# Optimization experiments

Hardware: AMD Instinct MI355X
Metric: run time of the kernel (lower is better)

The kernel has to match this reference:

```python
import jax, jax.numpy as jnp
import numpy as np

APERTURE = 256
IGNORE_ITSELF = False
FMAX = jnp.float32(3.4028235e38)  # tf.float32.max


def setup_inputs() -> dict:
    key = jax.random.key(0)
    ks = jax.random.split(key, 5)
    n, m, d = 4096, 1024, 1024
    scale = 1.0 / np.sqrt(m)
    x = jax.random.normal(ks[0], (n, m), dtype=jnp.float32)
    WK = jax.random.normal(ks[1], (m, d), dtype=jnp.float32) * scale
    WQ = jax.random.normal(ks[2], (m, d), dtype=jnp.float32) * scale
    WV = jax.random.normal(ks[3], (m, d), dtype=jnp.float32) * scale
    Wout = jax.random.normal(ks[4], (d, m), dtype=jnp.float32) * scale
    return {"x": x, "WK": WK, "WQ": WQ, "WV": WV, "Wout": Wout}


def reference(x, WK, WQ, WV, Wout):
    n = x.shape[0]
    K = x @ WK                      # [n, d]
    Q = (x @ WQ) * 0.06             # [n, d]
    V = x @ WV                      # [n, d]
    logits = Q @ K.T                # [n, n]

    i = jnp.arange(n)[:, None]
    j = jnp.arange(n)[None, :]
    if IGNORE_ITSELF:
        keep = (i != j).astype(jnp.float32)
        logits = logits * keep - FMAX * (1.0 - keep)
    if APERTURE > 0:
        # tf: mask = 1 - band_part(ones, -aperture, aperture); negative num_lower
        # keeps the whole lower triangle, so mask==1 exactly where j - i > aperture.
        keep = (j - i > APERTURE).astype(jnp.float32)
        logits = logits * keep - FMAX * (1.0 - keep)

    att_weights = jax.nn.softmax(logits, axis=-1)  # [n, n]
    # dropout is identity (training=False). NOTE faithful quirk: transpose_a=True.
    y = att_weights.T @ V           # [n, d]
    y = y @ Wout                    # [n, m]
    return (y, att_weights)
```

## Files before the change

### kernel.cpp

```cpp
#include <hip/hip_runtime.h>
#include <cstdint>
#include <cstddef>

#define N_TOK 4096
#define M_DIM 1024
#define APER  256
#define UNIF_START 3839

typedef __attribute__((ext_vector_type(8))) short short8;
typedef __attribute__((ext_vector_type(4))) float float4_t;

__device__ __forceinline__ unsigned short f2bf(float x) {
    union { float f; uint32_t u; } v; v.f = x;
    uint32_t u = v.u;
    u += 0x7FFFu + ((u >> 16) & 1u);
    return (unsigned short)(u >> 16);
}

__device__ __forceinline__ void gload16(const void* g, void* l) {
    __builtin_amdgcn_global_load_lds(
        (const __attribute__((address_space(1))) void*)g,
        (__attribute__((address_space(3))) void*)l, 16, 0, 0);
}

__global__ __launch_bounds__(256) void cast_bf16(const float* __restrict__ src,
                                                 unsigned short* __restrict__ dst, int n) {
    const int i = (blockIdx.x * 256 + threadIdx.x) * 4;
    if (i >= n) return;
    const float4 v = *reinterpret_cast<const float4*>(&src[i]);
    ushort4 o;
    o.x = f2bf(v.x); o.y = f2bf(v.y); o.z = f2bf(v.z); o.w = f2bf(v.w);
    *reinterpret_cast<ushort4*>(&dst[i]) = o;
}

__global__ __launch_bounds__(256) void wtrans3(const float* __restrict__ W0, const float* __restrict__ W1,
                                               const float* __restrict__ W2,
                                               unsigned short* __restrict__ D0, unsigned short* __restrict__ D1,
                                               unsigned short* __restrict__ D2) {
    const int z = blockIdx.z;
    const float* src = z == 0 ? W0 : (z == 1 ? W1 : W2);
    unsigned short* dst = z == 0 ? D0 : (z == 1 ? D1 : D2);
    __shared__ unsigned short tile[32][33];
    const int c0 = blockIdx.x * 32, r0 = blockIdx.y * 32;
    const int tx = threadIdx.x & 31, ty = threadIdx.x >> 5;
#pragma unroll
    for (int i = ty; i < 32; i += 8)
        tile[i][tx] = f2bf(src[(size_t)(r0 + i) * M_DIM + c0 + tx]);
    __syncthreads();
#pragma unroll
    for (int i = ty; i < 32; i += 8)
        dst[(size_t)(c0 + i) * M_DIM + r0 + tx] = tile[tx][i];
}

__global__ __launch_bounds__(256) void transpose_bf16(const unsigned short* __restrict__ src,
                                                      unsigned short* __restrict__ dst,
                                                      int R, int C) {
    __shared__ unsigned short tile[32][33];
    const int c0 = blockIdx.x * 32, r0 = blockIdx.y * 32;
    const int tx = threadIdx.x & 31, ty = threadIdx.x >> 5;
#pragma unroll
    for (int i = ty; i < 32; i += 8)
        tile[i][tx] = src[(size_t)(r0 + i) * C + c0 + tx];
    __syncthreads();
#pragma unroll
    for (int i = ty; i < 32; i += 8)
        dst[(size_t)(c0 + i) * R + r0 + tx] = tile[tx][i];
}

template <int SKIP>
__global__ __launch_bounds__(256) void nt64sq(const unsigned short* __restrict__ A,
                                              const unsigned short* __restrict__ B,
                                              float* __restrict__ Cf,
                                              unsigned short* __restrict__ Cb,
                                              int N, int K) {
    const int by   = (SKIP == 1) ? ((int)gridDim.y - 1 - (int)blockIdx.y) : (int)blockIdx.y;
    const int row0 = by * 64;
    const int col0 = blockIdx.x * 64;

    __shared__ unsigned short Asb[64 * 32];
    __shared__ unsigned short Bsb[64 * 32];

    const int t = threadIdx.x, w = t >> 6, lane = t & 63;
    float4_t acc[4] = {};

    const int sr   = lane >> 2;
    const int sk   = ((lane & 3) ^ ((sr >> 1) & 3)) * 8;
    const int m    = lane & 15;
    const int slot = ((lane >> 4) ^ ((m >> 1) & 3)) * 8;

    for (int k0 = 0; k0 < K; k0 += 32) {
        if (SKIP == 1) {
            if ((k0 > row0 + 63 - APER - 1) && (k0 + 31 < UNIF_START)) continue;
        }
        const int rr = w * 16 + sr;
        gload16(&A[(size_t)(row0 + rr) * K + k0 + sk], &Asb[w * 512]);
        gload16(&B[(size_t)(col0 + rr) * K + k0 + sk], &Bsb[w * 512]);
        __syncthreads();
        const short8 af = *reinterpret_cast<const short8*>(&Asb[(w * 16 + m) * 32 + slot]);
        short8 bf[4];
#pragma unroll
        for (int j = 0; j < 4; ++j)
            bf[j] = *reinterpret_cast<const short8*>(&Bsb[(j * 16 + m) * 32 + slot]);
#pragma unroll
        for (int j = 0; j < 4; ++j)
            acc[j] = __builtin_amdgcn_mfma_f32_16x16x32_bf16(af, bf[j], acc[j], 0, 0, 0);
        __syncthreads();
    }

    const int crow = row0 + w * 16 + (lane >> 4) * 4;
    const int ccol = col0 + m;
#pragma unroll
    for (int j = 0; j < 4; ++j)
#pragma unroll
        for (int r = 0; r < 4; ++r) {
            const float v = acc[j][r];
            const size_t idx = (size_t)(crow + r) * N + ccol + j * 16;
            if (Cf) Cf[idx] = v;
            if (Cb) Cb[idx] = f2bf(v);
        }
}

__global__ __launch_bounds__(256) void atv_db(const unsigned short* __restrict__ A,
                                              const unsigned short* __restrict__ B,
                                              float* __restrict__ C) {
    const int by   = (int)gridDim.y - 1 - (int)blockIdx.y;
    const int row0 = by * 64;
    const int col0 = blockIdx.x * 128;

    __shared__ unsigned short As[2][64 * 64];
    __shared__ unsigned short Bs[2][128 * 64];

    const int t = threadIdx.x, w = t >> 6, lane = t & 63;
    const int wr = (w >> 1) * 32, wc = (w & 1) * 64;
    const int q = lane >> 4, m = lane & 15;

    const int srow = lane >> 3;
    const int schk = ((lane & 7) ^ (srow & 7)) * 8;

    int aoff[2][2], boff[4][2];
#pragma unroll
    for (int i = 0; i < 2; ++i)
#pragma unroll
        for (int h = 0; h < 2; ++h)
            aoff[i][h] = (wr + i * 16 + m) * 64 + (((h * 4 + q) ^ (m & 7)) * 8);
#pragma unroll
    for (int j = 0; j < 4; ++j)
#pragma unroll
        for (int h = 0; h < 2; ++h)
            boff[j][h] = (wc + j * 16 + m) * 64 + (((h * 4 + q) ^ (m & 7)) * 8);

    const int limit = row0 - 194;
    int nPre = (limit >= 0) ? (limit / 64 + 1) : 0;
    if (nPre > 59) nPre = 59;
    const int nT = nPre + 5;

    float4_t acc[2][4] = {};

    auto kof = [&](int s) { return s < nPre ? s * 64 : 3776 + (s - nPre) * 64; };

    auto stage = [&](int buf, int k0) {
#pragma unroll
        for (int c = 0; c < 2; ++c) {
            const int r0 = w * 16 + c * 8;
            gload16(&A[(size_t)(row0 + r0 + srow) * (size_t)N_TOK + k0 + schk],
                    &As[buf][r0 * 64]);
        }
#pragma unroll
        for (int c = 0; c < 4; ++c) {
            const int r0 = w * 32 + c * 8;
            gload16(&B[(size_t)(col0 + r0 + srow) * (size_t)N_TOK + k0 + schk],
                    &Bs[buf][r0 * 64]);
        }
    };

    stage(0, kof(0));
    __syncthreads();

    int cur = 0;
    for (int s = 0; s < nT; ++s) {
        if (s + 1 < nT) stage(cur ^ 1, kof(s + 1));
        short8 af[2][2], bf[4][2];
#pragma unroll
        for (int i = 0; i < 2; ++i)
#pragma unroll
            for (int h = 0; h < 2; ++h)
                af[i][h] = *reinterpret_cast<const short8*>(&As[cur][aoff[i][h]]);
#pragma unroll
        for (int j = 0; j < 4; ++j)
#pragma unroll
            for (int h = 0; h < 2; ++h)
                bf[j][h] = *reinterpret_cast<const short8*>(&Bs[cur][boff[j][h]]);
#pragma unroll
        for (int i = 0; i < 2; ++i)
#pragma unroll
            for (int j = 0; j < 4; ++j)
#pragma unroll
                for (int h = 0; h < 2; ++h)
                    acc[i][j] = __builtin_amdgcn_mfma_f32_16x16x32_bf16(af[i][h], bf[j][h],
                                                                        acc[i][j], 0, 0, 0);
        __syncthreads();
        cur ^= 1;
    }

#pragma unroll
    for (int i = 0; i < 2; ++i)
#pragma unroll
        for (int j = 0; j < 4; ++j)
#pragma unroll
            for (int r = 0; r < 4; ++r)
                C[(size_t)(row0 + wr + i * 16 + q * 4 + r) * M_DIM + col0 + wc + j * 16 + m] =
                    acc[i][j][r];
}

__global__ __launch_bounds__(256) void mfma_qkv(const unsigned short* __restrict__ xb,
                                                const unsigned short* __restrict__ WKt,
                                                const unsigned short* __restrict__ WQt,
                                                const unsigned short* __restrict__ WVWt,
                                                unsigned short* __restrict__ Kb,
                                                unsigned short* __restrict__ Qb,
                                                unsigned short* __restrict__ VWb) {
    const int row0  = blockIdx.y * 128;
    const int col0g = blockIdx.x * 128;
    const int seg   = col0g >> 10;
    const int col0  = col0g & 1023;
    const unsigned short* B = seg == 0 ? WKt : (seg == 1 ? WQt : WVWt);
    unsigned short*       C = seg == 0 ? Kb  : (seg == 1 ? Qb  : VWb);
    const float alpha = (seg == 1) ? 0.06f : 1.0f;

    __shared__ unsigned short Asb[128 * 32];
    __shared__ unsigned short Bsb[128 * 32];

    const int t = threadIdx.x, w = t >> 6, lane = t & 63;
    const int wr = (w >> 1) * 64, wc = (w & 1) * 64;

    float4_t acc[4][4] = {};

    const int sr   = lane >> 2;
    const int sk   = ((lane & 3) ^ ((sr >> 1) & 3)) * 8;
    const int m    = lane & 15;
    const int slot = ((lane >> 4) ^ ((m >> 1) & 3)) * 8;

    for (int k0 = 0; k0 < M_DIM; k0 += 32) {
#pragma unroll
        for (int cc = 0; cc < 2; ++cc) {
            const int c = 2 * w + cc;
            const int rr = c * 16 + sr;
            gload16(&xb[(size_t)(row0 + rr) * M_DIM + k0 + sk], &Asb[c * 512]);
            gload16(&B[(size_t)(col0 + rr) * M_DIM + k0 + sk], &Bsb[c * 512]);
        }
        __syncthreads();
        short8 af[4], bf[4];
#pragma unroll
        for (int i = 0; i < 4; ++i)
            af[i] = *reinterpret_cast<const short8*>(&Asb[(wr + i * 16 + m) * 32 + slot]);
#pragma unroll
        for (int j = 0; j < 4; ++j)
            bf[j] = *reinterpret_cast<const short8*>(&Bsb[(wc + j * 16 + m) * 32 + slot]);
#pragma unroll
        for (int i = 0; i < 4; ++i)
#pragma unroll
            for (int j = 0; j < 4; ++j)
                acc[i][j] = __builtin_amdgcn_mfma_f32_16x16x32_bf16(af[i], bf[j], acc[i][j], 0, 0, 0);
        __syncthreads();
    }

    const int crow = row0 + wr + (lane >> 4) * 4;
    const int ccol = col0 + wc + m;
#pragma unroll
    for (int i = 0; i < 4; ++i)
#pragma unroll
        for (int j = 0; j < 4; ++j)
#pragma unroll
            for (int r = 0; r < 4; ++r)
                C[(size_t)(crow + i * 16 + r) * M_DIM + ccol + j * 16] = f2bf(alpha * acc[i][j][r]);
}

__global__ __launch_bounds__(256) void mfma_logits_exp(const unsigned short* __restrict__ A,
                                                       const unsigned short* __restrict__ B,
                                                       float* __restrict__ att,
                                                       float* __restrict__ rowsum) {
    const int row0 = blockIdx.y * 128;
    const int col0 = blockIdx.x * 128;
    if (col0 + 127 <= row0 + APER) return;

    __shared__ unsigned short Asb[128 * 32];
    __shared__ unsigned short Bsb[128 * 32];

    const int t = threadIdx.x, w = t >> 6, lane = t & 63;
    const int wr = (w >> 1) * 64, wc = (w & 1) * 64;

    float4_t acc[4][4] = {};

    const int sr   = lane >> 2;
    const int sk   = ((lane & 3) ^ ((sr >> 1) & 3)) * 8;
    const int m    = lane & 15;
    const int slot = ((lane >> 4) ^ ((m >> 1) & 3)) * 8;

    for (int k0 = 0; k0 < M_DIM; k0 += 32) {
#pragma unroll
        for (int cc = 0; cc < 2; ++cc) {
            const int c = 2 * w + cc;
            const int rr = c * 16 + sr;
            gload16(&A[(size_t)(row0 + rr) * M_DIM + k0 + sk], &Asb[c * 512]);
            gload16(&B[(size_t)(col0 + rr) * M_DIM + k0 + sk], &Bsb[c * 512]);
        }
        __syncthreads();
        short8 af[4], bf[4];
#pragma unroll
        for (int i = 0; i < 4; ++i)
            af[i] = *reinterpret_cast<const short8*>(&Asb[(wr + i * 16 + m) * 32 + slot]);
#pragma unroll
        for (int j = 0; j < 4; ++j)
            bf[j] = *reinterpret_cast<const short8*>(&Bsb[(wc + j * 16 + m) * 32 + slot]);
#pragma unroll
        for (int i = 0; i < 4; ++i)
#pragma unroll
            for (int j = 0; j < 4; ++j)
                acc[i][j] = __builtin_amdgcn_mfma_f32_16x16x32_bf16(af[i], bf[j], acc[i][j], 0, 0, 0);
        __syncthreads();
    }

    const int crow = row0 + wr + (lane >> 4) * 4;
    const int ccol = col0 + wc + m;
#pragma unroll
    for (int i = 0; i < 4; ++i) {
#pragma unroll
        for (int r = 0; r < 4; ++r) {
            const int gr = crow + i * 16 + r;
            float partial = 0.0f;
#pragma unroll
            for (int j = 0; j < 4; ++j) {
                const int gc = ccol + j * 16;
                float val;
                if (gr >= UNIF_START) {
                    val = 1.0f;
                } else if (gc > gr + APER) {
                    val = __expf(acc[i][j][r]);
                    partial += val;
                } else {
                    val = 0.0f;
                }
                att[(size_t)gr * N_TOK + gc] = val;
            }
            partial += __shfl_xor(partial, 1, 64);
            partial += __shfl_xor(partial, 2, 64);
            partial += __shfl_xor(partial, 4, 64);
            partial += __shfl_xor(partial, 8, 64);
            if (m == 0 && gr < UNIF_START) atomicAdd(&rowsum[gr], partial);
        }
    }
}

__global__ __launch_bounds__(256) void init_rowsum(float* __restrict__ rowsum) {
    const int i = blockIdx.x * 256 + threadIdx.x;
    if (i < N_TOK) rowsum[i] = (i >= UNIF_START) ? (float)N_TOK : 0.0f;
}

__global__ __launch_bounds__(256) void finalize_att(float* __restrict__ att,
                                                    unsigned short* __restrict__ attT,
                                                    const float* __restrict__ rowsum) {
    const int j0 = blockIdx.x * 64, i0 = blockIdx.y * 64;
    const int t = threadIdx.x;
    const int rl = t >> 4;
    const int c4 = (t & 15) * 4;
    const float u = 1.0f / (float)N_TOK;

    if (j0 + 63 <= i0 + APER) {
#pragma unroll
        for (int s = 0; s < 4; ++s) {
            const int i = i0 + rl + 16 * s;
            const float val = (i >= UNIF_START) ? u : 0.0f;
            float4 v; v.x = v.y = v.z = v.w = val;
            *reinterpret_cast<float4*>(&att[(size_t)i * N_TOK + j0 + c4]) = v;
        }
        const unsigned short bu = f2bf(u);
#pragma unroll
        for (int s = 0; s < 4; ++s) {
            const int j = j0 + rl + 16 * s;
            ushort4 o;
            o.x = (i0 + c4 + 0 >= UNIF_START) ? bu : 0;
            o.y = (i0 + c4 + 1 >= UNIF_START) ? bu : 0;
            o.z = (i0 + c4 + 2 >= UNIF_START) ? bu : 0;
            o.w = (i0 + c4 + 3 >= UNIF_START) ? bu : 0;
            *reinterpret_cast<ushort4*>(&attT[(size_t)j * N_TOK + i0 + c4]) = o;
        }
        return;
    }

    __shared__ unsigned short tile[64][72];
#pragma unroll
    for (int s = 0; s < 4; ++s) {
        const int il = rl + 16 * s;
        const int i  = i0 + il;
        const float inv = 1.0f / rowsum[i];
        float4 v = *reinterpret_cast<const float4*>(&att[(size_t)i * N_TOK + j0 + c4]);
        v.x *= inv; v.y *= inv; v.z *= inv; v.w *= inv;
        *reinterpret_cast<float4*>(&att[(size_t)i * N_TOK + j0 + c4]) = v;
        ushort4 b;
        b.x = f2bf(v.x); b.y = f2bf(v.y); b.z = f2bf(v.z); b.w = f2bf(v.w);
        *reinterpret_cast<ushort4*>(&tile[il][c4]) = b;
    }
    __syncthreads();
#pragma unroll
    for (int s = 0; s < 4; ++s) {
        const int jl = rl + 16 * s;
        ushort4 o;
        o.x = tile[c4 + 0][jl];
        o.y = tile[c4 + 1][jl];
        o.z = tile[c4 + 2][jl];
        o.w = tile[c4 + 3][jl];
        *reinterpret_cast<ushort4*>(&attT[(size_t)(j0 + jl) * N_TOK + i0 + c4]) = o;
    }
}

extern "C" void kernel_launch(void* const* d_in, const int* in_sizes, int n_in,
                              void* d_out, int out_size, void* d_ws, size_t ws_size,
                              hipStream_t stream) {
    const float* x    = (const float*)d_in[0];
    const float* WK   = (const float*)d_in[1];
    const float* WQ   = (const float*)d_in[2];
    const float* WV   = (const float*)d_in[3];
    const float* Wout = (const float*)d_in[4];

    float* y   = (float*)d_out;
    float* att = y + (size_t)N_TOK * M_DIM;

    unsigned short* base = (unsigned short*)d_ws;
    const size_t MEG = 1u << 20;
    unsigned short* xb    = base;
    unsigned short* WKt   = base + 4  * MEG;
    unsigned short* WQt   = base + 5  * MEG;
    unsigned short* Woutt = base + 6  * MEG;
    unsigned short* WVb   = base + 7  * MEG;
    unsigned short* WVWt  = base + 8  * MEG;
    unsigned short* Kb    = base + 9  * MEG;
    unsigned short* Qb    = base + 13 * MEG;
    unsigned short* VWb   = base + 17 * MEG;
    unsigned short* attT  = base + 4  * MEG;
    float*          rowsum = (float*)(base + 20 * MEG);
    unsigned short* VWt   = xb;

    const dim3 blk(256);

    cast_bf16<<<dim3((N_TOK * M_DIM) / 1024), blk, 0, stream>>>(x, xb, N_TOK * M_DIM);
    cast_bf16<<<dim3((M_DIM * M_DIM) / 1024), blk, 0, stream>>>(WV, WVb, M_DIM * M_DIM);
    wtrans3<<<dim3(M_DIM / 32, M_DIM / 32, 3), blk, 0, stream>>>(WK, WQ, Wout, WKt, WQt, Woutt);

    nt64sq<0><<<dim3(M_DIM / 64, M_DIM / 64), blk, 0, stream>>>(Woutt, WVb, nullptr, WVWt,
                                                                M_DIM, M_DIM);

    mfma_qkv<<<dim3(24, N_TOK / 128), blk, 0, stream>>>(xb, WKt, WQt, WVWt, Kb, Qb, VWb);

    transpose_bf16<<<dim3(M_DIM / 32, N_TOK / 32), blk, 0, stream>>>(VWb, VWt, N_TOK, M_DIM);

    init_rowsum<<<dim3(N_TOK / 256), blk, 0, stream>>>(rowsum);
    mfma_logits_exp<<<dim3(N_TOK / 128, N_TOK / 128), blk, 0, stream>>>(Qb, Kb, att, rowsum);

    finalize_att<<<dim3(N_TOK / 64, N_TOK / 64), blk, 0, stream>>>(att, attT, rowsum);

    atv_db<<<dim3(M_DIM / 128, N_TOK / 64), blk, 0, stream>>>(attT, VWt, y);
}
```

Baseline: 294.3 us.

## Double-buffer logits GEMM with 64x128 tiles and K-step of 64

```diff
diff --git a/kernel.cpp b/kernel.cpp
--- a/kernel.cpp
+++ b/kernel.cpp
@@ -212,125 +212,89 @@
                     acc[i][j][r];
 }
 
-__global__ __launch_bounds__(256) void mfma_qkv(const unsigned short* __restrict__ xb,
-                                                const unsigned short* __restrict__ WKt,
-                                                const unsigned short* __restrict__ WQt,
-                                                const unsigned short* __restrict__ WVWt,
-                                                unsigned short* __restrict__ Kb,
-                                                unsigned short* __restrict__ Qb,
-                                                unsigned short* __restrict__ VWb) {
-    const int row0  = blockIdx.y * 128;
-    const int col0g = blockIdx.x * 128;
-    const int seg   = col0g >> 10;
-    const int col0  = col0g & 1023;
-    const unsigned short* B = seg == 0 ? WKt : (seg == 1 ? WQt : WVWt);
-    unsigned short*       C = seg == 0 ? Kb  : (seg == 1 ? Qb  : VWb);
-    const float alpha = (seg == 1) ? 0.06f : 1.0f;
-
-    __shared__ unsigned short Asb[128 * 32];
-    __shared__ unsigned short Bsb[128 * 32];
-
-    const int t = threadIdx.x, w = t >> 6, lane = t & 63;
-    const int wr = (w >> 1) * 64, wc = (w & 1) * 64;
-
-    float4_t acc[4][4] = {};
-
-    const int sr   = lane >> 2;
-    const int sk   = ((lane & 3) ^ ((sr >> 1) & 3)) * 8;
-    const int m    = lane & 15;
-    const int slot = ((lane >> 4) ^ ((m >> 1) & 3)) * 8;
-
-    for (int k0 = 0; k0 < M_DIM; k0 += 32) {
-#pragma unroll
-        for (int cc = 0; cc < 2; ++cc) {
-            const int c = 2 * w + cc;
-            const int rr = c * 16 + sr;
-            gload16(&xb[(size_t)(row0 + rr) * M_DIM + k0 + sk], &Asb[c * 512]);
-            gload16(&B[(size_t)(col0 + rr) * M_DIM + k0 + sk], &Bsb[c * 512]);
-        }
-        __syncthreads();
-        short8 af[4], bf[4];
-#pragma unroll
-        for (int i = 0; i < 4; ++i)
-            af[i] = *reinterpret_cast<const short8*>(&Asb[(wr + i * 16 + m) * 32 + slot]);
-#pragma unroll
-        for (int j = 0; j < 4; ++j)
-            bf[j] = *reinterpret_cast<const short8*>(&Bsb[(wc + j * 16 + m) * 32 + slot]);
-#pragma unroll
-        for (int i = 0; i < 4; ++i)
-#pragma unroll
-            for (int j = 0; j < 4; ++j)
-                acc[i][j] = __builtin_amdgcn_mfma_f32_16x16x32_bf16(af[i], bf[j], acc[i][j], 0, 0, 0);
-        __syncthreads();
-    }
-
-    const int crow = row0 + wr + (lane >> 4) * 4;
-    const int ccol = col0 + wc + m;
-#pragma unroll
-    for (int i = 0; i < 4; ++i)
-#pragma unroll
-        for (int j = 0; j < 4; ++j)
-#pragma unroll
-            for (int r = 0; r < 4; ++r)
-                C[(size_t)(crow + i * 16 + r) * M_DIM + ccol + j * 16] = f2bf(alpha * acc[i][j][r]);
-}
-
-__global__ __launch_bounds__(256) void mfma_logits_exp(const unsigned short* __restrict__ A,
-                                                       const unsigned short* __restrict__ B,
-                                                       float* __restrict__ att,
-                                                       float* __restrict__ rowsum) {
-    const int row0 = blockIdx.y * 128;
+__global__ __launch_bounds__(256) void logits_db(const unsigned short* __restrict__ A,
+                                                 const unsigned short* __restrict__ B,
+                                                 float* __restrict__ att,
+                                                 float* __restrict__ rowsum) {
+    const int row0 = blockIdx.y * 64;
     const int col0 = blockIdx.x * 128;
     if (col0 + 127 <= row0 + APER) return;
 
-    __shared__ unsigned short Asb[128 * 32];
-    __shared__ unsigned short Bsb[128 * 32];
+    __shared__ unsigned short As[2][64 * 64];
+    __shared__ unsigned short Bs[2][128 * 64];
 
     const int t = threadIdx.x, w = t >> 6, lane = t & 63;
-    const int wr = (w >> 1) * 64, wc = (w & 1) * 64;
-
-    float4_t acc[4][4] = {};
-
-    const int sr   = lane >> 2;
-    const int sk   = ((lane & 3) ^ ((sr >> 1) & 3)) * 8;
-    const int m    = lane & 15;
-    const int slot = ((lane >> 4) ^ ((m >> 1) & 3)) * 8;
-
-    for (int k0 = 0; k0 < M_DIM; k0 += 32) {
-#pragma unroll
-        for (int cc = 0; cc < 2; ++cc) {
-            const int c = 2 * w + cc;
-            const int rr = c * 16 + sr;
-            gload16(&A[(size_t)(row0 + rr) * M_DIM + k0 + sk], &Asb[c * 512]);
-            gload16(&B[(size_t)(col0 + rr) * M_DIM + k0 + sk], &Bsb[c * 512]);
-        }
-        __syncthreads();
-        short8 af[4], bf[4];
-#pragma unroll
-        for (int i = 0; i < 4; ++i)
-            af[i] = *reinterpret_cast<const short8*>(&Asb[(wr + i * 16 + m) * 32 + slot]);
-#pragma unroll
-        for (int j = 0; j < 4; ++j)
-            bf[j] = *reinterpret_cast<const short8*>(&Bsb[(wc + j * 16 + m) * 32 + slot]);
-#pragma unroll
-        for (int i = 0; i < 4; ++i)
+    const int wr = (w >> 1) * 32, wc = (w & 1) * 64;
+    const int q = lane >> 4, m = lane & 15;
+
+    const int srow = lane >> 3;
+    const int schk = ((lane & 7) ^ (srow & 7)) * 8;
+
+    int aoff[2][2], boff[4][2];
+#pragma unroll
+    for (int i = 0; i < 2; ++i)
+#pragma unroll
+        for (int h = 0; h < 2; ++h)
+            aoff[i][h] = (wr + i * 16 + m) * 64 + (((h * 4 + q) ^ (m & 7)) * 8);
+#pragma unroll
+    for (int j = 0; j < 4; ++j)
+#pragma unroll
+        for (int h = 0; h < 2; ++h)
+            boff[j][h] = (wc + j * 16 + m) * 64 + (((h * 4 + q) ^ (m & 7)) * 8);
+
+    float4_t acc[2][4] = {};
+
+    auto stage = [&](int buf, int k0) {
+#pragma unroll
+        for (int c = 0; c < 2; ++c) {
+            const int r0 = w * 16 + c * 8;
+            gload16(&A[(size_t)(row0 + r0 + srow) * M_DIM + k0 + schk], &As[buf][r0 * 64]);
+        }
+#pragma unroll
+        for (int c = 0; c < 4; ++c) {
+            const int r0 = w * 32 + c * 8;
+            gload16(&B[(size_t)(col0 + r0 + srow) * M_DIM + k0 + schk], &Bs[buf][r0 * 64]);
+        }
+    };
+
+    stage(0, 0);
+    __syncthreads();
+
+    int cur = 0;
+    for (int s = 0; s < 16; ++s) {
+        if (s + 1 < 16) stage(cur ^ 1, (s + 1) * 64);
+        short8 af[2][2], bf[4][2];
+#pragma unroll
+        for (int i = 0; i < 2; ++i)
+#pragma unroll
+            for (int h = 0; h < 2; ++h)
+                af[i][h] = *reinterpret_cast<const short8*>(&As[cur][aoff[i][h]]);
+#pragma unroll
+        for (int j = 0; j < 4; ++j)
+#pragma unroll
+            for (int h = 0; h < 2; ++h)
+                bf[j][h] = *reinterpret_cast<const short8*>(&Bs[cur][boff[j][h]]);
+#pragma unroll
+        for (int i = 0; i < 2; ++i)
 #pragma unroll
             for (int j = 0; j < 4; ++j)
-                acc[i][j] = __builtin_amdgcn_mfma_f32_16x16x32_bf16(af[i], bf[j], acc[i][j], 0, 0, 0);
-        __syncthreads();
-    }
-
-    const int crow = row0 + wr + (lane >> 4) * 4;
-    const int ccol = col0 + wc + m;
-#pragma unroll
-    for (int i = 0; i < 4; ++i) {
+#pragma unroll
+                for (int h = 0; h < 2; ++h)
+                    acc[i][j] = __builtin_amdgcn_mfma_f32_16x16x32_bf16(af[i][h], bf[j][h],
+                                                                        acc[i][j], 0, 0, 0);
+        __syncthreads();
+        cur ^= 1;
+    }
+
+#pragma unroll
+    for (int i = 0; i < 2; ++i) {
 #pragma unroll
         for (int r = 0; r < 4; ++r) {
-            const int gr = crow + i * 16 + r;
+            const int gr = row0 + wr + i * 16 + q * 4 + r;
             float partial = 0.0f;
 #pragma unroll
             for (int j = 0; j < 4; ++j) {
-                const int gc = ccol + j * 16;
+                const int gc = col0 + wc + j * 16 + m;
                 float val;
                 if (gr >= UNIF_START) {
                     val = 1.0f;
@@ -351,6 +315,69 @@
     }
 }
 
+__global__ __launch_bounds__(256) void mfma_qkv(const unsigned short* __restrict__ xb,
+                                                const unsigned short* __restrict__ WKt,
+                                                const unsigned short* __restrict__ WQt,
+                                                const unsigned short* __restrict__ WVWt,
+                                                unsigned short* __restrict__ Kb,
+                                                unsigned short* __restrict__ Qb,
+                                                unsigned short* __restrict__ VWb) {
+    const int row0  = blockIdx.y * 128;
+    const int col0g = blockIdx.x * 128;
+    const int seg   = col0g >> 10;
+    const int col0  = col0g & 1023;
+    const unsigned short* B = seg == 0 ? WKt : (seg == 1 ? WQt : WVWt);
+    unsigned short*       C = seg == 0 ? Kb  : (seg == 1 ? Qb  : VWb);
+    const float alpha = (seg == 1) ? 0.06f : 1.0f;
+
+    __shared__ unsigned short Asb[128 * 32];
+    __shared__ unsigned short Bsb[128 * 32];
+
+    const int t = threadIdx.x, w = t >> 6, lane = t & 63;
+    const int wr = (w >> 1) * 64, wc = (w & 1) * 64;
+
+    float4_t acc[4][4] = {};
+
+    const int sr   = lane >> 2;
+    const int sk   = ((lane & 3) ^ ((sr >> 1) & 3)) * 8;
+    const int m    = lane & 15;
+    const int slot = ((lane >> 4) ^ ((m >> 1) & 3)) * 8;
+
+    for (int k0 = 0; k0 < M_DIM; k0 += 32) {
+#pragma unroll
+        for (int cc = 0; cc < 2; ++cc) {
+            const int c = 2 * w + cc;
+            const int rr = c * 16 + sr;
+            gload16(&xb[(size_t)(row0 + rr) * M_DIM + k0 + sk], &Asb[c * 512]);
+            gload16(&B[(size_t)(col0 + rr) * M_DIM + k0 + sk], &Bsb[c * 512]);
+        }
+        __syncthreads();
+        short8 af[4], bf[4];
+#pragma unroll
+        for (int i = 0; i < 4; ++i)
+            af[i] = *reinterpret_cast<const short8*>(&Asb[(wr + i * 16 + m) * 32 + slot]);
+#pragma unroll
+        for (int j = 0; j < 4; ++j)
+            bf[j] = *reinterpret_cast<const short8*>(&Bsb[(wc + j * 16 + m) * 32 + slot]);
+#pragma unroll
+        for (int i = 0; i < 4; ++i)
+#pragma unroll
+            for (int j = 0; j < 4; ++j)
+                acc[i][j] = __builtin_amdgcn_mfma_f32_16x16x32_bf16(af[i], bf[j], acc[i][j], 0, 0, 0);
+        __syncthreads();
+    }
+
+    const int crow = row0 + wr + (lane >> 4) * 4;
+    const int ccol = col0 + wc + m;
+#pragma unroll
+    for (int i = 0; i < 4; ++i)
+#pragma unroll
+        for (int j = 0; j < 4; ++j)
+#pragma unroll
+            for (int r = 0; r < 4; ++r)
+                C[(size_t)(crow + i * 16 + r) * M_DIM + ccol + j * 16] = f2bf(alpha * acc[i][j][r]);
+}
+
 __global__ __launch_bounds__(256) void init_rowsum(float* __restrict__ rowsum) {
     const int i = blockIdx.x * 256 + threadIdx.x;
     if (i < N_TOK) rowsum[i] = (i >= UNIF_START) ? (float)N_TOK : 0.0f;
@@ -454,7 +481,7 @@
     transpose_bf16<<<dim3(M_DIM / 32, N_TOK / 32), blk, 0, stream>>>(VWb, VWt, N_TOK, M_DIM);
 
     init_rowsum<<<dim3(N_TOK / 256), blk, 0, stream>>>(rowsum);
-    mfma_logits_exp<<<dim3(N_TOK / 128, N_TOK / 128), blk, 0, stream>>>(Qb, Kb, att, rowsum);
+    logits_db<<<dim3(N_TOK / 128, N_TOK / 64), blk, 0, stream>>>(Qb, Kb, att, rowsum);
 
     finalize_att<<<dim3(N_TOK / 64, N_TOK / 64), blk, 0, stream>>>(att, attT, rowsum);
 
```

After: 298.1 us. Within noise of the previous version (+1.3%).
